# Optimization experiments

Hardware: AMD Instinct MI355X
Metric: run time of the kernel (lower is better)

## Reference

```python
import jax, jax.numpy as jnp
import numpy as np

T, H, I, E, TOPK = 1024, 1024, 2048, 8, 2


def setup_inputs() -> dict:
    key = jax.random.key(0)
    k1, k2, k3, k4, k5, k6 = jax.random.split(key, 6)
    hidden_states = jax.random.normal(k1, (T, H), dtype=jnp.float32)
    expert_affinities = jax.random.uniform(k2, (T, E), dtype=jnp.float32)
    expert_index = jax.random.randint(k3, (T, TOPK), 0, E, dtype=jnp.int64)
    # Expert GLU MLP weights: gate/up [E,H,I], down [E,I,H]
    w_gate = jax.random.normal(k4, (E, H, I), dtype=jnp.float32) / np.sqrt(H)
    w_up = jax.random.normal(k5, (E, H, I), dtype=jnp.float32) / np.sqrt(H)
    w_down = jax.random.normal(k6, (E, I, H), dtype=jnp.float32) / np.sqrt(I)
    return {
        "hidden_states": hidden_states,
        "expert_affinities": expert_affinities,
        "expert_index": expert_index,
        "w_gate": w_gate,
        "w_up": w_up,
        "w_down": w_down,
        "seq_len": T,
    }


def reference(hidden_states, expert_affinities, expert_index, w_gate, w_up, w_down, seq_len):
    # Gather top-k affinities and renormalize (normalize_top_k_affinities=True)
    topk_aff = jnp.take_along_axis(expert_affinities, expert_index, axis=1)  # [T,K]
    topk_aff = topk_aff / jnp.sum(topk_aff, axis=1, keepdims=True)
    # Dense combine weights [T,E] (scatter of normalized top-k affinities)
    t_idx = jnp.arange(hidden_states.shape[0])[:, None]
    combine = jnp.zeros((hidden_states.shape[0], w_gate.shape[0]),
                        dtype=hidden_states.dtype).at[t_idx, expert_index].add(topk_aff)
    # GLU expert MLP for all experts (E small, grouped-GEMM form)
    g = jnp.einsum("th,ehi->tei", hidden_states, w_gate)  # [T,E,I]
    u = jnp.einsum("th,ehi->tei", hidden_states, w_up)    # [T,E,I]
    act = jax.nn.silu(g) * u                               # [T,E,I]
    # Down-projection fused with affinity-weighted combine
    out = jnp.einsum("tei,eih,te->th", act, w_down, combine)  # [T,H]
    return out
```

## Files before the change

### kernel.cpp

```cpp
#include <hip/hip_runtime.h>
#include <hip/hip_bf16.h>
#include <math.h>

#define T_ 1024
#define H_ 1024
#define I_ 2048
#define E_ 8
#define TOPK_ 2
#define NSLOT 2048

#define BM 128
#define BN 64
#define BK 32
#define CHUNKS_PER_E (NSLOT / BM)
#define SPLITK2 2

typedef __attribute__((ext_vector_type(8))) short bf16x8;
typedef __attribute__((ext_vector_type(4))) float f32x4;
typedef __attribute__((ext_vector_type(4))) unsigned uint4v;

__device__ __forceinline__ short f2bf(float f) {
  union { float f; unsigned u; } v; v.f = f;
  unsigned r = v.u + 0x7FFFu + ((v.u >> 16) & 1u);
  return (short)(r >> 16);
}
__device__ __forceinline__ unsigned cvtpk(float lo, float hi) {
  unsigned r;
  asm("v_cvt_pk_bf16_f32 %0, %1, %2" : "=v"(r) : "v"(lo), "v"(hi));
  return r;
}
__device__ __forceinline__ void gll16(const void* g, void* l) {
  __builtin_amdgcn_global_load_lds(
      (const __attribute__((address_space(1))) void*)g,
      (__attribute__((address_space(3))) void*)l, 16, 0, 0);
}

__device__ __forceinline__ unsigned bswz(int n, int kbyte) {
  return (unsigned)(n * 64 + (kbyte ^ (((n >> 2) & 3) << 4)));
}

__global__ __launch_bounds__(256) void k_prep(const float* __restrict__ hs,
                                              short* __restrict__ hs_bf) {
  int i = (blockIdx.x * 256 + threadIdx.x) * 8;
  float4 v0 = *(const float4*)&hs[i];
  float4 v1 = *(const float4*)&hs[i + 4];
  uint4v p;
  p.x = cvtpk(v0.x, v0.y); p.y = cvtpk(v0.z, v0.w);
  p.z = cvtpk(v1.x, v1.y); p.w = cvtpk(v1.z, v1.w);
  *(uint4v*)&hs_bf[i] = p;
}

__global__ __launch_bounds__(1024) void k_build(
    const float* __restrict__ aff, const int* __restrict__ eidx,
    int* __restrict__ offs, int* __restrict__ slot_tok, float* __restrict__ slot_w) {
  __shared__ int cnt[E_];
  __shared__ int soff[E_ + 1];
  int t = threadIdx.x;
  if (t < E_) cnt[t] = 0;
  __syncthreads();
  int e0 = eidx[t * 2 + 0];
  int e1 = eidx[t * 2 + 1];
  float a0 = aff[t * E_ + e0];
  float a1 = aff[t * E_ + e1];
  float inv = 1.0f / (a0 + a1);
  int r0 = atomicAdd(&cnt[e0], 1);
  int r1 = atomicAdd(&cnt[e1], 1);
  __syncthreads();
  if (t == 0) {
    int s = 0;
    for (int e = 0; e < E_; ++e) { soff[e] = s; s += cnt[e]; }
    soff[E_] = s;
  }
  __syncthreads();
  if (t <= E_) offs[t] = soff[t];
  int s0 = soff[e0] + r0;
  int s1 = soff[e1] + r1;
  slot_tok[s0] = t; slot_w[s0] = a0 * inv;
  slot_tok[s1] = t; slot_w[s1] = a1 * inv;
}

__global__ __launch_bounds__(512, 4) void k_gemm1(
    const short* __restrict__ hs_bf, const float* __restrict__ wg,
    const float* __restrict__ wu, const int* __restrict__ offs,
    const int* __restrict__ slot_tok, short* __restrict__ act) {
  int e = blockIdx.y >> 4;
  int chunk = blockIdx.y & (CHUNKS_PER_E - 1);
  int lo = offs[e], hi = offs[e + 1];
  int row0 = lo + chunk * BM;
  if (row0 >= hi) return;
  int rows = min(BM, hi - row0);
  int i0 = blockIdx.x * BN;

  __shared__ short sA[2][BM * BK];
  __shared__ short sB[2][2][BN * BK];

  int tid = threadIdx.x;
  int lane = tid & 63;
  int w = tid >> 6;
  int wm = w >> 1, wn = w & 1;
  int lr = lane & 15;
  int lk = (lane >> 4) * 8;

  const float* wgE = wg + (size_t)e * H_ * I_;
  const float* wuE = wu + (size_t)e * H_ * I_;

  int ra = 16 * w + (lane >> 2);
  int tokA = slot_tok[row0 + min(ra, rows - 1)];
  const short* srcA = hs_bf + (size_t)tokA * H_ + (lane & 3) * 8;
  const float* wB = (w < 4) ? wgE : wuE;
  int mat = (w >= 4);
  int up = 4 * (w & 3) + (lane >> 4);
  int n4 = (lane & 15) * 4;
  const float* srcB = wB + (size_t)(2 * up) * I_ + i0 + n4;

  f32x4 accg[2][2], accu[2][2];
#pragma unroll
  for (int mr = 0; mr < 2; ++mr)
#pragma unroll
    for (int nr = 0; nr < 2; ++nr) {
      accg[mr][nr] = (f32x4){0.f, 0.f, 0.f, 0.f};
      accu[mr][nr] = (f32x4){0.f, 0.f, 0.f, 0.f};
    }

  gll16(srcA, &sA[0][w * 512]);
  {
    float4 b0 = *(const float4*)srcB;
    float4 b1 = *(const float4*)(srcB + I_);
    const float* b0p = &b0.x; const float* b1p = &b1.x;
#pragma unroll
    for (int j = 0; j < 4; ++j)
      *(unsigned*)((char*)&sB[0][mat][0] + bswz(n4 + j, 4 * up)) = cvtpk(b0p[j], b1p[j]);
  }
  __syncthreads();

  int buf = 0;
  const int NT = H_ / BK;
  for (int t = 0; t < NT; ++t) {
    float4 b0, b1;
    int has_next = (t + 1 < NT);
    if (has_next) {
      int k1 = (t + 1) * BK;
      gll16(srcA + k1, &sA[buf ^ 1][w * 512]);
      b0 = *(const float4*)(srcB + (size_t)k1 * I_);
      b1 = *(const float4*)(srcB + (size_t)(k1 + 1) * I_);
    }
    bf16x8 a[2], bg[2], bu[2];
#pragma unroll
    for (int mr = 0; mr < 2; ++mr)
      a[mr] = *(const bf16x8*)&sA[buf][(wm * 32 + mr * 16 + lr) * BK + lk];
#pragma unroll
    for (int nr = 0; nr < 2; ++nr) {
      int col = wn * 32 + nr * 16 + lr;
      unsigned off = bswz(col, lk * 2);
      bg[nr] = *(const bf16x8*)((const char*)&sB[buf][0][0] + off);
      bu[nr] = *(const bf16x8*)((const char*)&sB[buf][1][0] + off);
    }
#pragma unroll
    for (int mr = 0; mr < 2; ++mr)
#pragma unroll
      for (int nr = 0; nr < 2; ++nr) {
        accg[mr][nr] = __builtin_amdgcn_mfma_f32_16x16x32_bf16(a[mr], bg[nr], accg[mr][nr], 0, 0, 0);
        accu[mr][nr] = __builtin_amdgcn_mfma_f32_16x16x32_bf16(a[mr], bu[nr], accu[mr][nr], 0, 0, 0);
      }
    if (has_next) {
      const float* b0p = &b0.x; const float* b1p = &b1.x;
#pragma unroll
      for (int j = 0; j < 4; ++j)
        *(unsigned*)((char*)&sB[buf ^ 1][mat][0] + bswz(n4 + j, 4 * up)) = cvtpk(b0p[j], b1p[j]);
    }
    __syncthreads();
    buf ^= 1;
  }

#pragma unroll
  for (int mr = 0; mr < 2; ++mr) {
#pragma unroll
    for (int r = 0; r < 4; ++r) {
      int m = wm * 32 + mr * 16 + (lane >> 4) * 4 + r;
      if (m < rows) {
#pragma unroll
        for (int nr = 0; nr < 2; ++nr) {
          float g = accg[mr][nr][r];
          float u = accu[mr][nr][r];
          float sg = 1.0f / (1.0f + __expf(-g));
          act[(size_t)(row0 + m) * I_ + i0 + wn * 32 + nr * 16 + lr] = f2bf(g * sg * u);
        }
      }
    }
  }
}

__global__ __launch_bounds__(512, 4) void k_gemm2(
    const short* __restrict__ act, const float* __restrict__ wd,
    const int* __restrict__ offs, const int* __restrict__ slot_tok,
    const float* __restrict__ slot_w, float* __restrict__ out) {
  int e = blockIdx.y >> 4;
  int chunk = blockIdx.y & (CHUNKS_PER_E - 1);
  int lo = offs[e], hi = offs[e + 1];
  int row0 = lo + chunk * BM;
  if (row0 >= hi) return;
  int rows = min(BM, hi - row0);
  int h0 = blockIdx.x * BN;
  int kbase = blockIdx.z * (I_ / SPLITK2);

  __shared__ short sA[2][BM * BK];
  __shared__ short sB[2][BN * BK];

  int tid = threadIdx.x;
  int lane = tid & 63;
  int w = tid >> 6;
  int wm = w >> 1, wn = w & 1;
  int lr = lane & 15;
  int lk = (lane >> 4) * 8;

  const float* wdE = wd + (size_t)e * I_ * H_;

  int ra = min(16 * w + (lane >> 2), rows - 1);
  const short* srcA = act + (size_t)(row0 + ra) * I_ + kbase + (lane & 3) * 8;
  int up = tid >> 5;
  int n2 = (tid & 31) * 2;
  const float* srcB = wdE + (size_t)(kbase + 2 * up) * H_ + h0 + n2;

  f32x4 acc[2][2];
#pragma unroll
  for (int mr = 0; mr < 2; ++mr)
#pragma unroll
    for (int nr = 0; nr < 2; ++nr)
      acc[mr][nr] = (f32x4){0.f, 0.f, 0.f, 0.f};

  gll16(srcA, &sA[0][w * 512]);
  {
    float2 r0 = *(const float2*)srcB;
    float2 r1 = *(const float2*)(srcB + H_);
    *(unsigned*)((char*)&sB[0][0] + bswz(n2, 4 * up))     = cvtpk(r0.x, r1.x);
    *(unsigned*)((char*)&sB[0][0] + bswz(n2 + 1, 4 * up)) = cvtpk(r0.y, r1.y);
  }
  __syncthreads();

  int buf = 0;
  const int NT = (I_ / SPLITK2) / BK;
  for (int t = 0; t < NT; ++t) {
    float2 r0, r1;
    int has_next = (t + 1 < NT);
    if (has_next) {
      int k1 = (t + 1) * BK;
      gll16(srcA + k1, &sA[buf ^ 1][w * 512]);
      r0 = *(const float2*)(srcB + (size_t)k1 * H_);
      r1 = *(const float2*)(srcB + (size_t)(k1 + 1) * H_);
    }
    bf16x8 a[2], b[2];
#pragma unroll
    for (int mr = 0; mr < 2; ++mr)
      a[mr] = *(const bf16x8*)&sA[buf][(wm * 32 + mr * 16 + lr) * BK + lk];
#pragma unroll
    for (int nr = 0; nr < 2; ++nr)
      b[nr] = *(const bf16x8*)((const char*)&sB[buf][0] + bswz(wn * 32 + nr * 16 + lr, lk * 2));
#pragma unroll
    for (int mr = 0; mr < 2; ++mr)
#pragma unroll
      for (int nr = 0; nr < 2; ++nr)
        acc[mr][nr] = __builtin_amdgcn_mfma_f32_16x16x32_bf16(a[mr], b[nr], acc[mr][nr], 0, 0, 0);
    if (has_next) {
      *(unsigned*)((char*)&sB[buf ^ 1][0] + bswz(n2, 4 * up))     = cvtpk(r0.x, r1.x);
      *(unsigned*)((char*)&sB[buf ^ 1][0] + bswz(n2 + 1, 4 * up)) = cvtpk(r0.y, r1.y);
    }
    __syncthreads();
    buf ^= 1;
  }

#pragma unroll
  for (int mr = 0; mr < 2; ++mr) {
#pragma unroll
    for (int r = 0; r < 4; ++r) {
      int m = wm * 32 + mr * 16 + (lane >> 4) * 4 + r;
      if (m < rows) {
        int gs = row0 + m;
        float wc = slot_w[gs];
        int tok = slot_tok[gs];
#pragma unroll
        for (int nr = 0; nr < 2; ++nr)
          atomicAdd(&out[(size_t)tok * H_ + h0 + wn * 32 + nr * 16 + lr],
                    acc[mr][nr][r] * wc);
      }
    }
  }
}

extern "C" void kernel_launch(void* const* d_in, const int* in_sizes, int n_in,
                              void* d_out, int out_size, void* d_ws, size_t ws_size,
                              hipStream_t stream) {
  const float* hs   = (const float*)d_in[0];
  const float* aff  = (const float*)d_in[1];
  const int*   eidx = (const int*)d_in[2];
  const float* wg   = (const float*)d_in[3];
  const float* wu   = (const float*)d_in[4];
  const float* wd   = (const float*)d_in[5];
  float* out = (float*)d_out;

  char* ws = (char*)d_ws;
  int*   offs     = (int*)ws;
  int*   slot_tok = (int*)(ws + 64);
  float* slot_w   = (float*)(ws + 64 + NSLOT * 4);
  short* hs_bf    = (short*)(ws + 64 + NSLOT * 8);
  short* act      = (short*)(ws + 64 + NSLOT * 8 + (size_t)T_ * H_ * 2);

  hipMemsetAsync(d_out, 0, (size_t)out_size * sizeof(float), stream);
  k_build<<<1, T_, 0, stream>>>(aff, eidx, offs, slot_tok, slot_w);
  k_prep<<<(T_ * H_) / (256 * 8), 256, 0, stream>>>(hs, hs_bf);
  k_gemm1<<<dim3(I_ / BN, E_ * CHUNKS_PER_E), 512, 0, stream>>>(hs_bf, wg, wu, offs, slot_tok, act);
  k_gemm2<<<dim3(H_ / BN, E_ * CHUNKS_PER_E, SPLITK2), 512, 0, stream>>>(act, wd, offs, slot_tok, slot_w, out);
}
```

Measured before the change: 111.1 us.

## Deepen GEMM prefetch to two stages with partial vmcnt waits and unrolled loop

Both expert GEMM kernels now prefetch two K-tiles ahead: a 4-buffer ring for the activation tile loaded via global_load_lds, and register double-buffering for the fp32 weight loads converted to bf16 in LDS. The full __syncthreads is replaced by a barrier that waits only until vmcnt(3), so the loads for later tiles stay in flight. The loop is unrolled by four with constant buffer indices. The aim is to hide global load latency behind MFMA work. In exchange it doubles sA LDS use and adds registers. The hand-tuned waitcnt count could let a tile be read before it lands if the compiler emits a different number of loads.

```diff
diff --git a/kernel.cpp b/kernel.cpp
--- a/kernel.cpp
+++ b/kernel.cpp
@@ -6,7 +6,6 @@
 #define H_ 1024
 #define I_ 2048
 #define E_ 8
-#define TOPK_ 2
 #define NSLOT 2048
 
 #define BM 128
@@ -19,6 +18,8 @@
 typedef __attribute__((ext_vector_type(4))) float f32x4;
 typedef __attribute__((ext_vector_type(4))) unsigned uint4v;
 
+#define MFMA_BF16 __builtin_amdgcn_mfma_f32_16x16x32_bf16
+
 __device__ __forceinline__ short f2bf(float f) {
   union { float f; unsigned u; } v; v.f = f;
   unsigned r = v.u + 0x7FFFu + ((v.u >> 16) & 1u);
@@ -33,6 +34,19 @@
   __builtin_amdgcn_global_load_lds(
       (const __attribute__((address_space(1))) void*)g,
       (__attribute__((address_space(3))) void*)l, 16, 0, 0);
+}
+
+__device__ __forceinline__ void pipe_barrier() {
+  __builtin_amdgcn_sched_barrier(0);
+  asm volatile("s_waitcnt vmcnt(3) lgkmcnt(0)" ::: "memory");
+  __builtin_amdgcn_s_barrier();
+  __builtin_amdgcn_sched_barrier(0);
+}
+__device__ __forceinline__ void drain_barrier() {
+  __builtin_amdgcn_sched_barrier(0);
+  asm volatile("s_waitcnt vmcnt(0) lgkmcnt(0)" ::: "memory");
+  __builtin_amdgcn_s_barrier();
+  __builtin_amdgcn_sched_barrier(0);
 }
 
 __device__ __forceinline__ unsigned bswz(int n, int kbyte) {
@@ -91,7 +105,7 @@
   int rows = min(BM, hi - row0);
   int i0 = blockIdx.x * BN;
 
-  __shared__ short sA[2][BM * BK];
+  __shared__ short sA[4][BM * BK];
   __shared__ short sB[2][2][BN * BK];
 
   int tid = threadIdx.x;
@@ -122,55 +136,67 @@
       accu[mr][nr] = (f32x4){0.f, 0.f, 0.f, 0.f};
     }
 
+  float4 bs[2][2];
+
   gll16(srcA, &sA[0][w * 512]);
+  bs[0][0] = *(const float4*)srcB;
+  bs[0][1] = *(const float4*)(srcB + I_);
+  gll16(srcA + BK, &sA[1][w * 512]);
+  bs[1][0] = *(const float4*)(srcB + (size_t)BK * I_);
+  bs[1][1] = *(const float4*)(srcB + (size_t)(BK + 1) * I_);
   {
-    float4 b0 = *(const float4*)srcB;
-    float4 b1 = *(const float4*)(srcB + I_);
-    const float* b0p = &b0.x; const float* b1p = &b1.x;
+    const float* p0 = (const float*)&bs[0][0];
+    const float* p1 = (const float*)&bs[0][1];
 #pragma unroll
     for (int j = 0; j < 4; ++j)
-      *(unsigned*)((char*)&sB[0][mat][0] + bswz(n4 + j, 4 * up)) = cvtpk(b0p[j], b1p[j]);
-  }
-  __syncthreads();
-
-  int buf = 0;
+      *(unsigned*)((char*)&sB[0][mat][0] + bswz(n4 + j, 4 * up)) = cvtpk(p0[j], p1[j]);
+  }
+  drain_barrier();
+
   const int NT = H_ / BK;
-  for (int t = 0; t < NT; ++t) {
-    float4 b0, b1;
-    int has_next = (t + 1 < NT);
-    if (has_next) {
-      int k1 = (t + 1) * BK;
-      gll16(srcA + k1, &sA[buf ^ 1][w * 512]);
-      b0 = *(const float4*)(srcB + (size_t)k1 * I_);
-      b1 = *(const float4*)(srcB + (size_t)(k1 + 1) * I_);
-    }
-    bf16x8 a[2], bg[2], bu[2];
-#pragma unroll
-    for (int mr = 0; mr < 2; ++mr)
-      a[mr] = *(const bf16x8*)&sA[buf][(wm * 32 + mr * 16 + lr) * BK + lk];
-#pragma unroll
-    for (int nr = 0; nr < 2; ++nr) {
-      int col = wn * 32 + nr * 16 + lr;
-      unsigned off = bswz(col, lk * 2);
-      bg[nr] = *(const bf16x8*)((const char*)&sB[buf][0][0] + off);
-      bu[nr] = *(const bf16x8*)((const char*)&sB[buf][1][0] + off);
-    }
-#pragma unroll
-    for (int mr = 0; mr < 2; ++mr)
-#pragma unroll
-      for (int nr = 0; nr < 2; ++nr) {
-        accg[mr][nr] = __builtin_amdgcn_mfma_f32_16x16x32_bf16(a[mr], bg[nr], accg[mr][nr], 0, 0, 0);
-        accu[mr][nr] = __builtin_amdgcn_mfma_f32_16x16x32_bf16(a[mr], bu[nr], accu[mr][nr], 0, 0, 0);
-      }
-    if (has_next) {
-      const float* b0p = &b0.x; const float* b1p = &b1.x;
-#pragma unroll
-      for (int j = 0; j < 4; ++j)
-        *(unsigned*)((char*)&sB[buf ^ 1][mat][0] + bswz(n4 + j, 4 * up)) = cvtpk(b0p[j], b1p[j]);
-    }
-    __syncthreads();
-    buf ^= 1;
-  }
+
+#define G1_ITER(U, base_) do {                                                 \
+    int t_ = (base_) + (U);                                                    \
+    if (t_ + 2 < NT) {                                                         \
+      int k2 = (t_ + 2) * BK;                                                  \
+      gll16(srcA + k2, &sA[((U) + 2) & 3][w * 512]);                           \
+      bs[(U) & 1][0] = *(const float4*)(srcB + (size_t)k2 * I_);               \
+      bs[(U) & 1][1] = *(const float4*)(srcB + (size_t)(k2 + 1) * I_);         \
+    }                                                                          \
+    bf16x8 a0 = *(const bf16x8*)&sA[(U)][(wm * 32 + lr) * BK + lk];            \
+    bf16x8 a1 = *(const bf16x8*)&sA[(U)][(wm * 32 + 16 + lr) * BK + lk];       \
+    unsigned off0 = bswz(wn * 32 + lr, lk * 2);                                \
+    unsigned off1 = bswz(wn * 32 + 16 + lr, lk * 2);                           \
+    bf16x8 bg0 = *(const bf16x8*)((const char*)&sB[(U) & 1][0][0] + off0);     \
+    bf16x8 bg1 = *(const bf16x8*)((const char*)&sB[(U) & 1][0][0] + off1);     \
+    bf16x8 bu0 = *(const bf16x8*)((const char*)&sB[(U) & 1][1][0] + off0);     \
+    bf16x8 bu1 = *(const bf16x8*)((const char*)&sB[(U) & 1][1][0] + off1);     \
+    accg[0][0] = MFMA_BF16(a0, bg0, accg[0][0], 0, 0, 0);                      \
+    accg[0][1] = MFMA_BF16(a0, bg1, accg[0][1], 0, 0, 0);                      \
+    accg[1][0] = MFMA_BF16(a1, bg0, accg[1][0], 0, 0, 0);                      \
+    accg[1][1] = MFMA_BF16(a1, bg1, accg[1][1], 0, 0, 0);                      \
+    accu[0][0] = MFMA_BF16(a0, bu0, accu[0][0], 0, 0, 0);                      \
+    accu[0][1] = MFMA_BF16(a0, bu1, accu[0][1], 0, 0, 0);                      \
+    accu[1][0] = MFMA_BF16(a1, bu0, accu[1][0], 0, 0, 0);                      \
+    accu[1][1] = MFMA_BF16(a1, bu1, accu[1][1], 0, 0, 0);                      \
+    if (t_ + 1 < NT) {                                                         \
+      const float* p0 = (const float*)&bs[((U) + 1) & 1][0];                   \
+      const float* p1 = (const float*)&bs[((U) + 1) & 1][1];                   \
+      _Pragma("unroll")                                                        \
+      for (int j = 0; j < 4; ++j)                                              \
+        *(unsigned*)((char*)&sB[((U) + 1) & 1][mat][0] + bswz(n4 + j, 4 * up)) \
+            = cvtpk(p0[j], p1[j]);                                             \
+    }                                                                          \
+    pipe_barrier();                                                            \
+  } while (0)
+
+  for (int base = 0; base < NT; base += 4) {
+    G1_ITER(0, base);
+    G1_ITER(1, base);
+    G1_ITER(2, base);
+    G1_ITER(3, base);
+  }
+#undef G1_ITER
 
 #pragma unroll
   for (int mr = 0; mr < 2; ++mr) {
@@ -203,7 +229,7 @@
   int h0 = blockIdx.x * BN;
   int kbase = blockIdx.z * (I_ / SPLITK2);
 
-  __shared__ short sA[2][BM * BK];
+  __shared__ short sA[4][BM * BK];
   __shared__ short sB[2][BN * BK];
 
   int tid = threadIdx.x;
@@ -228,45 +254,54 @@
     for (int nr = 0; nr < 2; ++nr)
       acc[mr][nr] = (f32x4){0.f, 0.f, 0.f, 0.f};
 
+  float2 bs[2][2];
+
   gll16(srcA, &sA[0][w * 512]);
-  {
-    float2 r0 = *(const float2*)srcB;
-    float2 r1 = *(const float2*)(srcB + H_);
-    *(unsigned*)((char*)&sB[0][0] + bswz(n2, 4 * up))     = cvtpk(r0.x, r1.x);
-    *(unsigned*)((char*)&sB[0][0] + bswz(n2 + 1, 4 * up)) = cvtpk(r0.y, r1.y);
-  }
-  __syncthreads();
-
-  int buf = 0;
+  bs[0][0] = *(const float2*)srcB;
+  bs[0][1] = *(const float2*)(srcB + H_);
+  gll16(srcA + BK, &sA[1][w * 512]);
+  bs[1][0] = *(const float2*)(srcB + (size_t)BK * H_);
+  bs[1][1] = *(const float2*)(srcB + (size_t)(BK + 1) * H_);
+  *(unsigned*)((char*)&sB[0][0] + bswz(n2, 4 * up))     = cvtpk(bs[0][0].x, bs[0][1].x);
+  *(unsigned*)((char*)&sB[0][0] + bswz(n2 + 1, 4 * up)) = cvtpk(bs[0][0].y, bs[0][1].y);
+  drain_barrier();
+
   const int NT = (I_ / SPLITK2) / BK;
-  for (int t = 0; t < NT; ++t) {
-    float2 r0, r1;
-    int has_next = (t + 1 < NT);
-    if (has_next) {
-      int k1 = (t + 1) * BK;
-      gll16(srcA + k1, &sA[buf ^ 1][w * 512]);
-      r0 = *(const float2*)(srcB + (size_t)k1 * H_);
-      r1 = *(const float2*)(srcB + (size_t)(k1 + 1) * H_);
-    }
-    bf16x8 a[2], b[2];
-#pragma unroll
-    for (int mr = 0; mr < 2; ++mr)
-      a[mr] = *(const bf16x8*)&sA[buf][(wm * 32 + mr * 16 + lr) * BK + lk];
-#pragma unroll
-    for (int nr = 0; nr < 2; ++nr)
-      b[nr] = *(const bf16x8*)((const char*)&sB[buf][0] + bswz(wn * 32 + nr * 16 + lr, lk * 2));
-#pragma unroll
-    for (int mr = 0; mr < 2; ++mr)
-#pragma unroll
-      for (int nr = 0; nr < 2; ++nr)
-        acc[mr][nr] = __builtin_amdgcn_mfma_f32_16x16x32_bf16(a[mr], b[nr], acc[mr][nr], 0, 0, 0);
-    if (has_next) {
-      *(unsigned*)((char*)&sB[buf ^ 1][0] + bswz(n2, 4 * up))     = cvtpk(r0.x, r1.x);
-      *(unsigned*)((char*)&sB[buf ^ 1][0] + bswz(n2 + 1, 4 * up)) = cvtpk(r0.y, r1.y);
-    }
-    __syncthreads();
-    buf ^= 1;
-  }
+
+#define G2_ITER(U, base_) do {                                                 \
+    int t_ = (base_) + (U);                                                    \
+    if (t_ + 2 < NT) {                                                         \
+      int k2 = (t_ + 2) * BK;                                                  \
+      gll16(srcA + k2, &sA[((U) + 2) & 3][w * 512]);                           \
+      bs[(U) & 1][0] = *(const float2*)(srcB + (size_t)k2 * H_);               \
+      bs[(U) & 1][1] = *(const float2*)(srcB + (size_t)(k2 + 1) * H_);         \
+    }                                                                          \
+    bf16x8 a0 = *(const bf16x8*)&sA[(U)][(wm * 32 + lr) * BK + lk];            \
+    bf16x8 a1 = *(const bf16x8*)&sA[(U)][(wm * 32 + 16 + lr) * BK + lk];       \
+    bf16x8 b0 = *(const bf16x8*)((const char*)&sB[(U) & 1][0]                  \
+                                 + bswz(wn * 32 + lr, lk * 2));                \
+    bf16x8 b1 = *(const bf16x8*)((const char*)&sB[(U) & 1][0]                  \
+                                 + bswz(wn * 32 + 16 + lr, lk * 2));           \
+    acc[0][0] = MFMA_BF16(a0, b0, acc[0][0], 0, 0, 0);                         \
+    acc[0][1] = MFMA_BF16(a0, b1, acc[0][1], 0, 0, 0);                         \
+    acc[1][0] = MFMA_BF16(a1, b0, acc[1][0], 0, 0, 0);                         \
+    acc[1][1] = MFMA_BF16(a1, b1, acc[1][1], 0, 0, 0);                         \
+    if (t_ + 1 < NT) {                                                         \
+      *(unsigned*)((char*)&sB[((U) + 1) & 1][0] + bswz(n2, 4 * up))            \
+          = cvtpk(bs[((U) + 1) & 1][0].x, bs[((U) + 1) & 1][1].x);             \
+      *(unsigned*)((char*)&sB[((U) + 1) & 1][0] + bswz(n2 + 1, 4 * up))        \
+          = cvtpk(bs[((U) + 1) & 1][0].y, bs[((U) + 1) & 1][1].y);             \
+    }                                                                          \
+    pipe_barrier();                                                            \
+  } while (0)
+
+  for (int base = 0; base < NT; base += 4) {
+    G2_ITER(0, base);
+    G2_ITER(1, base);
+    G2_ITER(2, base);
+    G2_ITER(3, base);
+  }
+#undef G2_ITER
 
 #pragma unroll
   for (int mr = 0; mr < 2; ++mr) {
```

Measured after the change: 105.5 us. 5.0% less time.
